# Kernel optimization log

Measured on AMD Instinct MI355X. Metric: run time of the kernel, lower is better.

## Reference

```python
import jax, jax.numpy as jnp
import numpy as np

N_NODES = 100000
IN_DIM = 256
OUT_DIM = 128
N_EDGES = 3200000


def setup_inputs() -> dict:
    key = jax.random.key(0)
    k1, k2, k3, k4, k5, k6 = jax.random.split(key, 6)
    stdv = 1.0 / np.sqrt(OUT_DIM)
    return {
        "feature_map": jax.random.normal(k1, (N_NODES, IN_DIM), dtype=jnp.float32),
        "edge_src": jax.random.randint(k2, (N_EDGES,), 0, N_NODES, dtype=jnp.int32),
        "edge_dst": jax.random.randint(k3, (N_EDGES,), 0, N_NODES, dtype=jnp.int32),
        "edge_vals": jax.random.uniform(k4, (N_EDGES,), dtype=jnp.float32),
        "weights": jax.random.uniform(k5, (IN_DIM, OUT_DIM), dtype=jnp.float32, minval=-stdv, maxval=stdv),
        "b": jax.random.uniform(k6, (OUT_DIM,), dtype=jnp.float32, minval=-stdv, maxval=stdv),
    }


def reference(feature_map, edge_src, edge_dst, edge_vals, weights, b):
    # dense feature transform: [N, in] @ [in, out] -> [N, out]
    h = feature_map @ weights
    # sparse adjacency matmul A @ h via edge list:
    # out[dst] += A[dst, src] * h[src]
    msgs = edge_vals[:, None] * h[edge_src]  # [E, out]
    out = jax.ops.segment_sum(msgs, edge_dst, num_segments=N_NODES)
    # fused bias add epilogue
    return out + b
```

## Files before the change

kernel.cpp:

```cpp
#include <hip/hip_runtime.h>

#define N_NODES 100000
#define IN_DIM 256
#define OUT_DIM 128
#define N_EDGES 3200000

#define NB 1563
#define CAP 2560
#define PTILE 12800
#define PBLK 250

typedef __attribute__((ext_vector_type(8))) short short8;
typedef __attribute__((ext_vector_type(4))) float float4v;

__device__ __forceinline__ unsigned short f2bf(float f) {
    union { float f; unsigned int u; } v; v.f = f;
    unsigned int r = v.u + 0x7FFF + ((v.u >> 16) & 1);
    return (unsigned short)(r >> 16);
}

__global__ __launch_bounds__(256) void wconv_kernel(const float* __restrict__ W,
                                                    unsigned short* __restrict__ Wf) {
    const int f = blockIdx.x * 256 + threadIdx.x;
    const int lane = f & 63;
    const int qc = f >> 6;
    const int q = qc >> 3, ct = qc & 7;
    const int n = ct * 16 + (lane & 15);
    const int k0 = q * 32 + (lane >> 4) * 8;
    unsigned int o[4];
#pragma unroll
    for (int jj = 0; jj < 4; ++jj) {
        const unsigned short lo = f2bf(W[(k0 + 2 * jj) * OUT_DIM + n]);
        const unsigned short hi = f2bf(W[(k0 + 2 * jj + 1) * OUT_DIM + n]);
        o[jj] = (unsigned)lo | ((unsigned)hi << 16);
    }
    ((uint4*)Wf)[f] = make_uint4(o[0], o[1], o[2], o[3]);
}

__global__ __launch_bounds__(256) void gemm_kernel(const float* __restrict__ X,
                                                   const unsigned short* __restrict__ Wf,
                                                   unsigned short* __restrict__ hb) {
    const int tid = threadIdx.x;
    const int wid = tid >> 6;
    const int lane = tid & 63;
    const int m = lane & 15;
    const int quad = lane >> 4;
    const int row0 = blockIdx.x * 64 + wid * 16;

    const int rl = min(row0 + m, N_NODES - 1);
    const float* xr = X + (long)rl * IN_DIM + quad * 8;
    short8 afrag[8];
#pragma unroll
    for (int q = 0; q < 8; ++q) {
        const float4 xa = *(const float4*)(xr + q * 32);
        const float4 xb = *(const float4*)(xr + q * 32 + 4);
        short8 f;
        f[0] = (short)f2bf(xa.x); f[1] = (short)f2bf(xa.y);
        f[2] = (short)f2bf(xa.z); f[3] = (short)f2bf(xa.w);
        f[4] = (short)f2bf(xb.x); f[5] = (short)f2bf(xb.y);
        f[6] = (short)f2bf(xb.z); f[7] = (short)f2bf(xb.w);
        afrag[q] = f;
    }

    const short8* wfrag = (const short8*)Wf;
#pragma unroll 1
    for (int ct = 0; ct < 8; ++ct) {
        float4v acc = {0.f, 0.f, 0.f, 0.f};
#pragma unroll
        for (int q = 0; q < 8; ++q) {
            const short8 bfr = wfrag[(q * 8 + ct) * 64 + lane];
            acc = __builtin_amdgcn_mfma_f32_16x16x32_bf16(afrag[q], bfr, acc, 0, 0, 0);
        }
        const int col = ct * 16 + m;
#pragma unroll
        for (int r = 0; r < 4; ++r) {
            const int row = row0 + quad * 4 + r;
            if (row < N_NODES)
                hb[(long)row * OUT_DIM + col] = f2bf(acc[r]);
        }
    }
}

__global__ __launch_bounds__(256) void zero_cursor_kernel(int* __restrict__ cursor) {
    const int i = blockIdx.x * 256 + threadIdx.x;
    if (i < NB) cursor[i] = 0;
}

__global__ __launch_bounds__(512) void partition_kernel(const int* __restrict__ src,
                                                        const int* __restrict__ dst,
                                                        const float* __restrict__ vals,
                                                        int* __restrict__ cursor,
                                                        int2* __restrict__ pairs) {
    __shared__ int lhist[NB];
    __shared__ int lbase[NB];
    const int tid = threadIdx.x;
    const int base = blockIdx.x * PTILE;

    for (int i = tid; i < NB; i += 512) lhist[i] = 0;
    __syncthreads();

#pragma unroll 5
    for (int k = 0; k < PTILE / 512; ++k)
        atomicAdd(&lhist[dst[base + tid + k * 512] >> 6], 1);
    __syncthreads();

    for (int i = tid; i < NB; i += 512) {
        const int c = lhist[i];
        if (c) lbase[i] = atomicAdd(&cursor[i], c);
    }
    __syncthreads();
    for (int i = tid; i < NB; i += 512) lhist[i] = 0;
    __syncthreads();

#pragma unroll 5
    for (int k = 0; k < PTILE / 512; ++k) {
        const int e = base + tid + k * 512;
        const int d = dst[e];
        const int b = d >> 6;
        const int r = atomicAdd(&lhist[b], 1);
        const int pos = lbase[b] + r;
        if (pos < CAP)
            pairs[(long)b * CAP + pos] =
                make_int2(src[e] | ((d & 63) << 20), __float_as_int(vals[e]));
    }
}

__global__ __launch_bounds__(256) void gather_kernel(const int* __restrict__ cursor,
                                                     const int2* __restrict__ pairs,
                                                     const unsigned short* __restrict__ hb,
                                                     const float* __restrict__ bias,
                                                     float* __restrict__ out) {
    __shared__ int2 lp[CAP];
    __shared__ int rcnt[64];
    __shared__ int rbase[64];
    const int blk = blockIdx.x;
    const int tid = threadIdx.x;
    const int wid = tid >> 6;
    const int lane = tid & 63;
    const int c = lane * 2;

    const long beg = (long)blk * CAP;
    const int cnt = min(cursor[blk], CAP);

    if (tid < 64) rcnt[tid] = 0;
    __syncthreads();

    int2 sp[10];
    int  sr[10];
#pragma unroll
    for (int k = 0; k < 10; ++k) {
        const int i = tid + k * 256;
        sr[k] = -1;
        if (i < cnt) {
            const int2 p = pairs[beg + i];
            const int r = (p.x >> 20) & 63;
            const int rk = atomicAdd(&rcnt[r], 1);
            sp[k] = p;
            sr[k] = (r << 13) | rk;
        }
    }
    __syncthreads();

    if (wid == 0) {
        const int v = rcnt[lane];
        int incl = v;
#pragma unroll
        for (int off = 1; off < 64; off <<= 1) {
            const int t = __shfl_up(incl, off);
            if (lane >= off) incl += t;
        }
        rbase[lane] = incl - v;
    }
    __syncthreads();

#pragma unroll
    for (int k = 0; k < 10; ++k) {
        if (sr[k] >= 0)
            lp[rbase[sr[k] >> 13] + (sr[k] & 0x1FFF)] = sp[k];
    }
    __syncthreads();

    const float2 bb = *(const float2*)(bias + c);
#pragma unroll 1
    for (int rr = 0; rr < 16; ++rr) {
        const int r = wid * 16 + rr;
        const int node = blk * 64 + r;
        if (node >= N_NODES) break;
        const int rb = rbase[r];
        const int re = rb + rcnt[r];

        float2 a0 = make_float2(0.f, 0.f), a1 = make_float2(0.f, 0.f);
        float2 a2 = make_float2(0.f, 0.f), a3 = make_float2(0.f, 0.f);
        int j = rb;
        for (; j + 3 < re; j += 4) {
            const int2 p0 = lp[j],     p1 = lp[j + 1];
            const int2 p2 = lp[j + 2], p3 = lp[j + 3];
            const unsigned u0 = *(const unsigned*)(hb + (long)(p0.x & 0xFFFFF) * OUT_DIM + c);
            const unsigned u1 = *(const unsigned*)(hb + (long)(p1.x & 0xFFFFF) * OUT_DIM + c);
            const unsigned u2 = *(const unsigned*)(hb + (long)(p2.x & 0xFFFFF) * OUT_DIM + c);
            const unsigned u3 = *(const unsigned*)(hb + (long)(p3.x & 0xFFFFF) * OUT_DIM + c);
            const float v0 = __int_as_float(p0.y), v1 = __int_as_float(p1.y);
            const float v2 = __int_as_float(p2.y), v3 = __int_as_float(p3.y);
            a0.x += v0 * __uint_as_float(u0 << 16);
            a0.y += v0 * __uint_as_float(u0 & 0xFFFF0000u);
            a1.x += v1 * __uint_as_float(u1 << 16);
            a1.y += v1 * __uint_as_float(u1 & 0xFFFF0000u);
            a2.x += v2 * __uint_as_float(u2 << 16);
            a2.y += v2 * __uint_as_float(u2 & 0xFFFF0000u);
            a3.x += v3 * __uint_as_float(u3 << 16);
            a3.y += v3 * __uint_as_float(u3 & 0xFFFF0000u);
        }
        for (; j < re; ++j) {
            const int2 p0 = lp[j];
            const unsigned u0 = *(const unsigned*)(hb + (long)(p0.x & 0xFFFFF) * OUT_DIM + c);
            const float v0 = __int_as_float(p0.y);
            a0.x += v0 * __uint_as_float(u0 << 16);
            a0.y += v0 * __uint_as_float(u0 & 0xFFFF0000u);
        }
        float2 o;
        o.x = bb.x + (a0.x + a1.x) + (a2.x + a3.x);
        o.y = bb.y + (a0.y + a1.y) + (a2.y + a3.y);
        *(float2*)(out + (long)node * OUT_DIM + c) = o;
    }
}

extern "C" void kernel_launch(void* const* d_in, const int* in_sizes, int n_in,
                              void* d_out, int out_size, void* d_ws, size_t ws_size,
                              hipStream_t stream) {
    const float* X     = (const float*)d_in[0];
    const int*   esrc  = (const int*)d_in[1];
    const int*   edst  = (const int*)d_in[2];
    const float* evals = (const float*)d_in[3];
    const float* W     = (const float*)d_in[4];
    const float* b     = (const float*)d_in[5];
    float* out = (float*)d_out;

    char* ws = (char*)d_ws;
    unsigned short* hb = (unsigned short*)(ws);
    int2* pairs        = (int2*)(ws + 25600000);
    int*  cursor       = (int*) (ws + 25600000 + 32010240);
    unsigned short* Wf = (unsigned short*)(ws + 57616496);

    wconv_kernel<<<dim3(16), dim3(256), 0, stream>>>(W, Wf);
    zero_cursor_kernel<<<dim3((NB + 255) / 256), dim3(256), 0, stream>>>(cursor);
    partition_kernel<<<dim3(PBLK), dim3(512), 0, stream>>>(esrc, edst, evals, cursor, pairs);
    gemm_kernel<<<dim3((N_NODES + 63) / 64), dim3(256), 0, stream>>>(X, Wf, hb);
    gather_kernel<<<dim3(NB), dim3(256), 0, stream>>>(cursor, pairs, hb, b, out);
}
```

Before: 398.7 us.

## Fuse partition and GEMM into one launch, stage GEMM stores, deepen gather unroll

Merges weight conversion and cursor zeroing into a single setup kernel. Partition and the bf16 GEMM now run as disjoint block ranges of one kernel, so the two independent stages can overlap on the GPU instead of running back to back. The GEMM blocks grow to 128 rows and stage their output tile in LDS so each row is written with coalesced 16-byte stores, where before they were scattered 2-byte stores. The gather loop is unrolled to 8 independent loads and accumulators to expose more memory parallelism, at the cost of extra registers.

```diff
diff --git a/kernel.cpp b/kernel.cpp
--- a/kernel.cpp
+++ b/kernel.cpp
@@ -7,8 +7,9 @@
 
 #define NB 1563
 #define CAP 2560
-#define PTILE 12800
-#define PBLK 250
+#define PTILE 6400
+#define PBLK 500
+#define GBLK 782
 
 typedef __attribute__((ext_vector_type(8))) short short8;
 typedef __attribute__((ext_vector_type(4))) float float4v;
@@ -19,109 +20,123 @@
     return (unsigned short)(r >> 16);
 }
 
-__global__ __launch_bounds__(256) void wconv_kernel(const float* __restrict__ W,
-                                                    unsigned short* __restrict__ Wf) {
-    const int f = blockIdx.x * 256 + threadIdx.x;
-    const int lane = f & 63;
-    const int qc = f >> 6;
-    const int q = qc >> 3, ct = qc & 7;
-    const int n = ct * 16 + (lane & 15);
-    const int k0 = q * 32 + (lane >> 4) * 8;
-    unsigned int o[4];
-#pragma unroll
-    for (int jj = 0; jj < 4; ++jj) {
-        const unsigned short lo = f2bf(W[(k0 + 2 * jj) * OUT_DIM + n]);
-        const unsigned short hi = f2bf(W[(k0 + 2 * jj + 1) * OUT_DIM + n]);
-        o[jj] = (unsigned)lo | ((unsigned)hi << 16);
-    }
-    ((uint4*)Wf)[f] = make_uint4(o[0], o[1], o[2], o[3]);
-}
-
-__global__ __launch_bounds__(256) void gemm_kernel(const float* __restrict__ X,
-                                                   const unsigned short* __restrict__ Wf,
-                                                   unsigned short* __restrict__ hb) {
+__global__ __launch_bounds__(256) void setup_kernel(const float* __restrict__ W,
+                                                    unsigned short* __restrict__ Wf,
+                                                    int* __restrict__ cursor) {
+    if (blockIdx.x < 16) {
+        const int f = blockIdx.x * 256 + threadIdx.x;
+        const int lane = f & 63;
+        const int qc = f >> 6;
+        const int q = qc >> 3, ct = qc & 7;
+        const int n = ct * 16 + (lane & 15);
+        const int k0 = q * 32 + (lane >> 4) * 8;
+        unsigned int o[4];
+#pragma unroll
+        for (int jj = 0; jj < 4; ++jj) {
+            const unsigned short lo = f2bf(W[(k0 + 2 * jj) * OUT_DIM + n]);
+            const unsigned short hi = f2bf(W[(k0 + 2 * jj + 1) * OUT_DIM + n]);
+            o[jj] = (unsigned)lo | ((unsigned)hi << 16);
+        }
+        ((uint4*)Wf)[f] = make_uint4(o[0], o[1], o[2], o[3]);
+    } else {
+        const int i = (blockIdx.x - 16) * 256 + threadIdx.x;
+        if (i < NB) cursor[i] = 0;
+    }
+}
+
+__global__ __launch_bounds__(512, 4) void fused_kernel(const float* __restrict__ X,
+                                                       const unsigned short* __restrict__ Wf,
+                                                       unsigned short* __restrict__ hb,
+                                                       const int* __restrict__ src,
+                                                       const int* __restrict__ dst,
+                                                       const float* __restrict__ vals,
+                                                       int* __restrict__ cursor,
+                                                       int2* __restrict__ pairs) {
+    __shared__ int smem[8192];
     const int tid = threadIdx.x;
-    const int wid = tid >> 6;
-    const int lane = tid & 63;
-    const int m = lane & 15;
-    const int quad = lane >> 4;
-    const int row0 = blockIdx.x * 64 + wid * 16;
-
-    const int rl = min(row0 + m, N_NODES - 1);
-    const float* xr = X + (long)rl * IN_DIM + quad * 8;
-    short8 afrag[8];
-#pragma unroll
-    for (int q = 0; q < 8; ++q) {
-        const float4 xa = *(const float4*)(xr + q * 32);
-        const float4 xb = *(const float4*)(xr + q * 32 + 4);
-        short8 f;
-        f[0] = (short)f2bf(xa.x); f[1] = (short)f2bf(xa.y);
-        f[2] = (short)f2bf(xa.z); f[3] = (short)f2bf(xa.w);
-        f[4] = (short)f2bf(xb.x); f[5] = (short)f2bf(xb.y);
-        f[6] = (short)f2bf(xb.z); f[7] = (short)f2bf(xb.w);
-        afrag[q] = f;
-    }
-
-    const short8* wfrag = (const short8*)Wf;
+
+    if (blockIdx.x < PBLK) {
+        int* lhist = smem;
+        int* lbase = smem + NB;
+        const int base = blockIdx.x * PTILE;
+        const int lim = base + PTILE;
+
+        for (int i = tid; i < NB; i += 512) lhist[i] = 0;
+        __syncthreads();
+
+#pragma unroll
+        for (int k = 0; k < 13; ++k) {
+            const int e = base + tid + k * 512;
+            if (e < lim) atomicAdd(&lhist[dst[e] >> 6], 1);
+        }
+        __syncthreads();
+
+        for (int i = tid; i < NB; i += 512) {
+            const int c = lhist[i];
+            if (c) lbase[i] = atomicAdd(&cursor[i], c);
+        }
+        __syncthreads();
+        for (int i = tid; i < NB; i += 512) lhist[i] = 0;
+        __syncthreads();
+
+#pragma unroll
+        for (int k = 0; k < 13; ++k) {
+            const int e = base + tid + k * 512;
+            if (e < lim) {
+                const int d = dst[e];
+                const int b = d >> 6;
+                const int r = atomicAdd(&lhist[b], 1);
+                const int pos = lbase[b] + r;
+                if (pos < CAP)
+                    pairs[(long)b * CAP + pos] =
+                        make_int2(src[e] | ((d & 63) << 20), __float_as_int(vals[e]));
+            }
+        }
+    } else {
+        const int bid = blockIdx.x - PBLK;
+        const int wid = tid >> 6;
+        const int lane = tid & 63;
+        const int m = lane & 15;
+        const int quad = lane >> 4;
+        const int row0 = bid * 128 + wid * 16;
+
+        const int rl = min(row0 + m, N_NODES - 1);
+        const float* xr = X + (long)rl * IN_DIM + quad * 8;
+        short8 afrag[8];
+#pragma unroll
+        for (int q = 0; q < 8; ++q) {
+            const float4 xa = *(const float4*)(xr + q * 32);
+            const float4 xb = *(const float4*)(xr + q * 32 + 4);
+            short8 f;
+            f[0] = (short)f2bf(xa.x); f[1] = (short)f2bf(xa.y);
+            f[2] = (short)f2bf(xa.z); f[3] = (short)f2bf(xa.w);
+            f[4] = (short)f2bf(xb.x); f[5] = (short)f2bf(xb.y);
+            f[6] = (short)f2bf(xb.z); f[7] = (short)f2bf(xb.w);
+            afrag[q] = f;
+        }
+
+        unsigned short* stage = (unsigned short*)smem + wid * 2048;
+        const short8* wfrag = (const short8*)Wf;
 #pragma unroll 1
-    for (int ct = 0; ct < 8; ++ct) {
-        float4v acc = {0.f, 0.f, 0.f, 0.f};
-#pragma unroll
-        for (int q = 0; q < 8; ++q) {
-            const short8 bfr = wfrag[(q * 8 + ct) * 64 + lane];
-            acc = __builtin_amdgcn_mfma_f32_16x16x32_bf16(afrag[q], bfr, acc, 0, 0, 0);
-        }
-        const int col = ct * 16 + m;
-#pragma unroll
-        for (int r = 0; r < 4; ++r) {
-            const int row = row0 + quad * 4 + r;
-            if (row < N_NODES)
-                hb[(long)row * OUT_DIM + col] = f2bf(acc[r]);
-        }
-    }
-}
-
-__global__ __launch_bounds__(256) void zero_cursor_kernel(int* __restrict__ cursor) {
-    const int i = blockIdx.x * 256 + threadIdx.x;
-    if (i < NB) cursor[i] = 0;
-}
-
-__global__ __launch_bounds__(512) void partition_kernel(const int* __restrict__ src,
-                                                        const int* __restrict__ dst,
-                                                        const float* __restrict__ vals,
-                                                        int* __restrict__ cursor,
-                                                        int2* __restrict__ pairs) {
-    __shared__ int lhist[NB];
-    __shared__ int lbase[NB];
-    const int tid = threadIdx.x;
-    const int base = blockIdx.x * PTILE;
-
-    for (int i = tid; i < NB; i += 512) lhist[i] = 0;
-    __syncthreads();
-
-#pragma unroll 5
-    for (int k = 0; k < PTILE / 512; ++k)
-        atomicAdd(&lhist[dst[base + tid + k * 512] >> 6], 1);
-    __syncthreads();
-
-    for (int i = tid; i < NB; i += 512) {
-        const int c = lhist[i];
-        if (c) lbase[i] = atomicAdd(&cursor[i], c);
-    }
-    __syncthreads();
-    for (int i = tid; i < NB; i += 512) lhist[i] = 0;
-    __syncthreads();
-
-#pragma unroll 5
-    for (int k = 0; k < PTILE / 512; ++k) {
-        const int e = base + tid + k * 512;
-        const int d = dst[e];
-        const int b = d >> 6;
-        const int r = atomicAdd(&lhist[b], 1);
-        const int pos = lbase[b] + r;
-        if (pos < CAP)
-            pairs[(long)b * CAP + pos] =
-                make_int2(src[e] | ((d & 63) << 20), __float_as_int(vals[e]));
+        for (int ct = 0; ct < 8; ++ct) {
+            float4v acc = {0.f, 0.f, 0.f, 0.f};
+#pragma unroll
+            for (int q = 0; q < 8; ++q) {
+                const short8 bfr = wfrag[(q * 8 + ct) * 64 + lane];
+                acc = __builtin_amdgcn_mfma_f32_16x16x32_bf16(afrag[q], bfr, acc, 0, 0, 0);
+            }
+#pragma unroll
+            for (int r = 0; r < 4; ++r)
+                stage[(quad * 4 + r) * 128 + ct * 16 + m] = f2bf(acc[r]);
+        }
+
+#pragma unroll
+        for (int j = 0; j < 4; ++j) {
+            const uint4 vdata = *(const uint4*)(stage + j * 512 + lane * 8);
+            const int row_r = row0 + j * 4 + quad;
+            if (row_r < N_NODES)
+                *(uint4*)(hb + (long)row_r * OUT_DIM + m * 8) = vdata;
+        }
     }
 }
 
@@ -189,37 +204,38 @@
         const int rb = rbase[r];
         const int re = rb + rcnt[r];
 
-        float2 a0 = make_float2(0.f, 0.f), a1 = make_float2(0.f, 0.f);
-        float2 a2 = make_float2(0.f, 0.f), a3 = make_float2(0.f, 0.f);
+        float2 acc[8];
+#pragma unroll
+        for (int t = 0; t < 8; ++t) acc[t] = make_float2(0.f, 0.f);
+
         int j = rb;
-        for (; j + 3 < re; j += 4) {
-            const int2 p0 = lp[j],     p1 = lp[j + 1];
-            const int2 p2 = lp[j + 2], p3 = lp[j + 3];
-            const unsigned u0 = *(const unsigned*)(hb + (long)(p0.x & 0xFFFFF) * OUT_DIM + c);
-            const unsigned u1 = *(const unsigned*)(hb + (long)(p1.x & 0xFFFFF) * OUT_DIM + c);
-            const unsigned u2 = *(const unsigned*)(hb + (long)(p2.x & 0xFFFFF) * OUT_DIM + c);
-            const unsigned u3 = *(const unsigned*)(hb + (long)(p3.x & 0xFFFFF) * OUT_DIM + c);
-            const float v0 = __int_as_float(p0.y), v1 = __int_as_float(p1.y);
-            const float v2 = __int_as_float(p2.y), v3 = __int_as_float(p3.y);
-            a0.x += v0 * __uint_as_float(u0 << 16);
-            a0.y += v0 * __uint_as_float(u0 & 0xFFFF0000u);
-            a1.x += v1 * __uint_as_float(u1 << 16);
-            a1.y += v1 * __uint_as_float(u1 & 0xFFFF0000u);
-            a2.x += v2 * __uint_as_float(u2 << 16);
-            a2.y += v2 * __uint_as_float(u2 & 0xFFFF0000u);
-            a3.x += v3 * __uint_as_float(u3 << 16);
-            a3.y += v3 * __uint_as_float(u3 & 0xFFFF0000u);
+        for (; j + 7 < re; j += 8) {
+            int2 p[8];
+            unsigned u[8];
+#pragma unroll
+            for (int t = 0; t < 8; ++t) p[t] = lp[j + t];
+#pragma unroll
+            for (int t = 0; t < 8; ++t)
+                u[t] = *(const unsigned*)(hb + (long)(p[t].x & 0xFFFFF) * OUT_DIM + c);
+#pragma unroll
+            for (int t = 0; t < 8; ++t) {
+                const float v = __int_as_float(p[t].y);
+                acc[t].x += v * __uint_as_float(u[t] << 16);
+                acc[t].y += v * __uint_as_float(u[t] & 0xFFFF0000u);
+            }
         }
         for (; j < re; ++j) {
             const int2 p0 = lp[j];
             const unsigned u0 = *(const unsigned*)(hb + (long)(p0.x & 0xFFFFF) * OUT_DIM + c);
             const float v0 = __int_as_float(p0.y);
-            a0.x += v0 * __uint_as_float(u0 << 16);
-            a0.y += v0 * __uint_as_float(u0 & 0xFFFF0000u);
+            acc[0].x += v0 * __uint_as_float(u0 << 16);
+            acc[0].y += v0 * __uint_as_float(u0 & 0xFFFF0000u);
         }
         float2 o;
-        o.x = bb.x + (a0.x + a1.x) + (a2.x + a3.x);
-        o.y = bb.y + (a0.y + a1.y) + (a2.y + a3.y);
+        o.x = bb.x + ((acc[0].x + acc[1].x) + (acc[2].x + acc[3].x))
+                   + ((acc[4].x + acc[5].x) + (acc[6].x + acc[7].x));
+        o.y = bb.y + ((acc[0].y + acc[1].y) + (acc[2].y + acc[3].y))
+                   + ((acc[4].y + acc[5].y) + (acc[6].y + acc[7].y));
         *(float2*)(out + (long)node * OUT_DIM + c) = o;
     }
 }
@@ -241,9 +257,9 @@
     int*  cursor       = (int*) (ws + 25600000 + 32010240);
     unsigned short* Wf = (unsigned short*)(ws + 57616496);
 
-    wconv_kernel<<<dim3(16), dim3(256), 0, stream>>>(W, Wf);
-    zero_cursor_kernel<<<dim3((NB + 255) / 256), dim3(256), 0, stream>>>(cursor);
-    partition_kernel<<<dim3(PBLK), dim3(512), 0, stream>>>(esrc, edst, evals, cursor, pairs);
-    gemm_kernel<<<dim3((N_NODES + 63) / 64), dim3(256), 0, stream>>>(X, Wf, hb);
+    setup_kernel<<<dim3(23), dim3(256), 0, stream>>>(W, Wf, cursor);
+    fused_kernel<<<dim3(PBLK + GBLK), dim3(512), 0, stream>>>(X, Wf, hb,
+                                                              esrc, edst, evals,
+                                                              cursor, pairs);
     gather_kernel<<<dim3(NB), dim3(256), 0, stream>>>(cursor, pairs, hb, b, out);
 }
```

Result: no change. 397.8 us (-0.2%).
